# Optimization experiments

Measured on AMD Instinct MI355X. Metric: run time of the kernel, lower is better.

Reference implementation:

```python
import jax, jax.numpy as jnp
import numpy as np

B, N = 1, 1024
C_A, C_Z, H = 768, 128, 16
CH = C_A // H  # 48
INV_SQRT_CH = float(1.0 / np.sqrt(CH))


def _ln(x, w, b):
    # torch.nn.LayerNorm over last dim, eps=1e-5
    m = jnp.mean(x, axis=-1, keepdims=True)
    v = jnp.mean(jnp.square(x - m), axis=-1, keepdims=True)
    return (x - m) * jax.lax.rsqrt(v + 1e-5) * w + b


def setup_inputs() -> dict:
    key = jax.random.key(0)
    ks = jax.random.split(key, 8)
    rn = lambda k, shape, sc: jax.random.normal(k, shape, dtype=jnp.float32) * sc
    return {
        "a": rn(ks[0], (B, N, C_A), 1.0),
        "z": rn(ks[1], (B, N, N, C_Z), 1.0),
        "mask": jnp.ones((B, N), dtype=jnp.float32),
        "ln_a_w": jnp.ones((C_A,), jnp.float32),
        "ln_a_b": jnp.zeros((C_A,), jnp.float32),
        "ln_z_w": jnp.ones((C_Z,), jnp.float32),
        "ln_z_b": jnp.zeros((C_Z,), jnp.float32),
        "Wq": rn(ks[2], (C_A, H * CH), 0.02),
        "bq": jnp.zeros((H * CH,), jnp.float32),
        "Wk": rn(ks[3], (C_A, H * CH), 0.02),
        "Wv": rn(ks[4], (C_A, H * CH), 0.02),
        "Wb": rn(ks[5], (C_Z, H), 0.02),
        "Wg": rn(ks[6], (C_A, H * CH), 0.02),
        "Wo": rn(ks[7], (H * CH, C_A), 0.02),
    }


def reference(a, z, mask, ln_a_w, ln_a_b, ln_z_w, ln_z_b, Wq, bq, Wk, Wv, Wb, Wg, Wo):
    an = _ln(a, ln_a_w, ln_a_b)                                  # [B, N, C_A]
    q = (an @ Wq + bq).reshape(B, N, H, CH)
    k = (an @ Wk).reshape(B, N, H, CH)
    v = (an @ Wv).reshape(B, N, H, CH)
    # pair bias: LayerNorm(z) -> per-head scalar bias [B, N, N, H]
    bpair = _ln(z, ln_z_w, ln_z_b) @ Wb
    mbias = (mask - 1.0)[:, None, None, :] * 1e9                  # [B, 1, 1, N]
    logits = jnp.einsum('bqhc,bkhc->bhqk', q, k) * INV_SQRT_CH
    logits = logits + jnp.transpose(bpair, (0, 3, 1, 2)) + mbias  # [B, H, N, N]
    attn = jax.nn.softmax(logits, axis=-1)
    o = jnp.einsum('bhqk,bkhc->bqhc', attn, v)                    # [B, N, H, CH]
    g = jax.nn.sigmoid(an @ Wg).reshape(B, N, H, CH)
    out = (g * o).reshape(B, N, H * CH) @ Wo                      # [B, N, C_A]
    return out
```

## Files before the change

kernel.cpp:

```cpp
#include <hip/hip_runtime.h>

#define NSEQ 1024
#define CA   768
#define CZ   128
#define NH   16
#define CHD  48
#define HC   768
#define INV_SQRT_CH 0.14433756729740643f

typedef float v4f __attribute__((ext_vector_type(4)));
typedef short v8s __attribute__((ext_vector_type(8)));

__device__ __forceinline__ short f2bf(float f) {
  union { float f; unsigned u; } v; v.f = f;
  unsigned r = v.u + 0x7fffu + ((v.u >> 16) & 1u);
  return (short)(r >> 16);
}
__device__ __forceinline__ float bf2f(short s) {
  union { unsigned u; float f; } v;
  v.u = ((unsigned)(unsigned short)s) << 16;
  return v.f;
}
__device__ __forceinline__ unsigned cvtpk(float lo, float hi) {
  unsigned r;
  asm("v_cvt_pk_bf16_f32 %0, %1, %2" : "=v"(r) : "v"(lo), "v"(hi));
  return r;
}

__global__ __launch_bounds__(256) void k_front(
    const float* __restrict__ lnzw, const float* __restrict__ lnzb,
    const float* __restrict__ Wb, short* __restrict__ wWp, float* __restrict__ S1bW,
    const float* __restrict__ Wq, const float* __restrict__ Wk,
    const float* __restrict__ Wv, const float* __restrict__ Wg,
    const float* __restrict__ Wo, short* __restrict__ WT, short* __restrict__ WoT,
    const float* __restrict__ a, const float* __restrict__ lnaw,
    const float* __restrict__ lnab, short* __restrict__ anb)
{
  __shared__ __align__(16) char fsm[64 * 65 * 4];
  const int bid = blockIdx.x;
  const int t = threadIdx.x;

  if (bid == 0) {
    const int s = t >> 6, l = t & 63;
    const int r16 = l & 15, cg = l >> 4;
    float v[8];
    #pragma unroll
    for (int j = 0; j < 8; ++j) {
      int d = s * 32 + cg * 8 + j;
      v[j] = lnzw[d] * Wb[d * NH + r16];
    }
    uint4 pk;
    pk.x = cvtpk(v[0], v[1]); pk.y = cvtpk(v[2], v[3]);
    pk.z = cvtpk(v[4], v[5]); pk.w = cvtpk(v[6], v[7]);
    *(uint4*)(wWp + (s * 64 + l) * 8) = pk;
    if (t < NH) {
      float s1 = 0.f, bw = 0.f;
      for (int d = 0; d < CZ; ++d) {
        float wb = Wb[d * NH + t];
        s1 += bf2f(f2bf(lnzw[d] * wb));
        bw += lnzb[d] * wb;
      }
      S1bW[t] = s1;
      S1bW[NH + t] = bw;
    }
  } else if (bid <= 720) {
    float (*tile)[65] = (float(*)[65])fsm;
    const int cb = bid - 1;
    const int mat = cb / 144, rem = cb % 144;
    const int tk = rem % 12, tn = rem / 12;
    const int k0 = tk * 64, n0 = tn * 64;
    const float* __restrict__ W =
        (mat == 0) ? Wq : (mat == 1) ? Wk : (mat == 2) ? Wv : (mat == 3) ? Wg : Wo;
    const float s = (mat == 0) ? INV_SQRT_CH : 1.f;
    const int rr = t >> 4, cc = (t & 15) * 4;
    #pragma unroll
    for (int r = 0; r < 4; ++r) {
      v4f v = *(const v4f*)(W + (size_t)(k0 + r * 16 + rr) * HC + n0 + cc);
      tile[r * 16 + rr][cc + 0] = v[0];
      tile[r * 16 + rr][cc + 1] = v[1];
      tile[r * 16 + rr][cc + 2] = v[2];
      tile[r * 16 + rr][cc + 3] = v[3];
    }
    __syncthreads();
    short* dst = (mat < 4) ? (WT + (size_t)mat * HC * CA) : WoT;
    #pragma unroll
    for (int r = 0; r < 4; ++r) {
      const int nr = r * 16 + rr;
      uint2 pk;
      pk.x = cvtpk(tile[cc + 0][nr] * s, tile[cc + 1][nr] * s);
      pk.y = cvtpk(tile[cc + 2][nr] * s, tile[cc + 3][nr] * s);
      *(uint2*)(dst + (size_t)(n0 + nr) * CA + k0 + cc) = pk;
    }
  } else {
    float* red = (float*)fsm;
    const int row = bid - 721;
    const float* ar = a + (size_t)row * CA;
    float x[3];
    float s = 0.f, s2 = 0.f;
    #pragma unroll
    for (int i = 0; i < 3; ++i) {
      x[i] = ar[t + i * 256];
      s += x[i]; s2 += x[i] * x[i];
    }
    #pragma unroll
    for (int off = 1; off < 64; off <<= 1) {
      s += __shfl_xor(s, off);
      s2 += __shfl_xor(s2, off);
    }
    const int wv = t >> 6;
    if ((t & 63) == 0) { red[wv] = s; red[4 + wv] = s2; }
    __syncthreads();
    s = red[0] + red[1] + red[2] + red[3];
    s2 = red[4] + red[5] + red[6] + red[7];
    const float m = s * (1.f / CA);
    const float var = s2 * (1.f / CA) - m * m;
    const float rs = rsqrtf(var + 1e-5f);
    #pragma unroll
    for (int i = 0; i < 3; ++i) {
      int c = t + i * 256;
      anb[(size_t)row * CA + c] = f2bf((x[i] - m) * rs * lnaw[c] + lnab[c]);
    }
  }
}

__global__ __launch_bounds__(256) void k2_gemm(
    const short* __restrict__ anb, const short* __restrict__ WT,
    const float* __restrict__ bq,
    short* __restrict__ qb, short* __restrict__ kb, short* __restrict__ vT,
    float* __restrict__ gbuf)
{
  __shared__ __align__(16) short As[128 * 40];
  __shared__ __align__(16) short Bs[128 * 40];
  const int tid = threadIdx.x;
  const int w = tid >> 6, l = tid & 63;
  const int r16 = l & 15, cg = l >> 4;
  const int bm = blockIdx.x & 7;
  const int bnb = blockIdx.x >> 3;
  const int m0 = bm * 128, n0 = bnb * 128;
  const int wr = w >> 1, wc = w & 1;
  const int strow = w * 16 + (l >> 2);
  const int scol = (l & 3) * 8;

  v4f acc[4][4];
  #pragma unroll
  for (int i = 0; i < 4; ++i)
    #pragma unroll
    for (int j = 0; j < 4; ++j)
      acc[i][j] = (v4f){0.f, 0.f, 0.f, 0.f};

  for (int k0 = 0; k0 < CA; k0 += 32) {
    v8s av0 = *(const v8s*)(anb + (size_t)(m0 + strow) * CA + k0 + scol);
    v8s av1 = *(const v8s*)(anb + (size_t)(m0 + 64 + strow) * CA + k0 + scol);
    v8s bv0 = *(const v8s*)(WT + (size_t)(n0 + strow) * CA + k0 + scol);
    v8s bv1 = *(const v8s*)(WT + (size_t)(n0 + 64 + strow) * CA + k0 + scol);
    __syncthreads();
    *(v8s*)(As + (size_t)strow * 40 + scol) = av0;
    *(v8s*)(As + (size_t)(64 + strow) * 40 + scol) = av1;
    *(v8s*)(Bs + (size_t)strow * 40 + scol) = bv0;
    *(v8s*)(Bs + (size_t)(64 + strow) * 40 + scol) = bv1;
    __syncthreads();
    v8s a[4], b[4];
    #pragma unroll
    for (int m = 0; m < 4; ++m)
      a[m] = *(const v8s*)(As + (wr * 64 + m * 16 + r16) * 40 + cg * 8);
    #pragma unroll
    for (int n = 0; n < 4; ++n)
      b[n] = *(const v8s*)(Bs + (wc * 64 + n * 16 + r16) * 40 + cg * 8);
    #pragma unroll
    for (int m = 0; m < 4; ++m)
      #pragma unroll
      for (int n = 0; n < 4; ++n)
        acc[m][n] = __builtin_amdgcn_mfma_f32_16x16x32_bf16(a[m], b[n], acc[m][n], 0, 0, 0);
  }

  const int matsel = n0 / HC;
  #pragma unroll
  for (int n = 0; n < 4; ++n) {
    const int nc = (n0 % HC) + wc * 64 + n * 16 + r16;
    const int rbase = m0 + wr * 64 + cg * 4;
    if (matsel == 0) {
      const float bqs = bq[nc] * INV_SQRT_CH;
      #pragma unroll
      for (int m = 0; m < 4; ++m)
        #pragma unroll
        for (int j = 0; j < 4; ++j)
          qb[(size_t)(rbase + m * 16 + j) * HC + nc] = f2bf(acc[m][n][j] + bqs);
    } else if (matsel == 1) {
      #pragma unroll
      for (int m = 0; m < 4; ++m)
        #pragma unroll
        for (int j = 0; j < 4; ++j)
          kb[(size_t)(rbase + m * 16 + j) * HC + nc] = f2bf(acc[m][n][j]);
    } else if (matsel == 2) {
      #pragma unroll
      for (int m = 0; m < 4; ++m) {
        uint2 pk;
        pk.x = cvtpk(acc[m][n][0], acc[m][n][1]);
        pk.y = cvtpk(acc[m][n][2], acc[m][n][3]);
        *(uint2*)(vT + (size_t)nc * NSEQ + rbase + m * 16) = pk;
      }
    } else {
      #pragma unroll
      for (int m = 0; m < 4; ++m)
        #pragma unroll
        for (int j = 0; j < 4; ++j)
          gbuf[(size_t)(rbase + m * 16 + j) * HC + nc] =
              1.f / (1.f + __expf(-acc[m][n][j]));
    }
  }
}

__global__ __launch_bounds__(256) void k3_z(
    const float* __restrict__ z, const short* __restrict__ wWp,
    const float* __restrict__ S1bW, short* __restrict__ bpair)
{
  __shared__ __align__(16) short blds[16 * 72];
  const int tid = threadIdx.x;
  const int w = tid >> 6, l = tid & 63;
  const int r16 = l & 15, cg = l >> 4;
  const int q = blockIdx.x >> 4;
  const int k0 = (blockIdx.x & 15) << 6;

  v8s bfrag[4];
  #pragma unroll
  for (int s = 0; s < 4; ++s) bfrag[s] = *(const v8s*)(wWp + (s * 64 + l) * 8);
  const float S1 = S1bW[r16];
  const float bW = S1bW[NH + r16];

  const int krow = k0 + w * 16 + r16;
  const float* __restrict__ zr = z + ((size_t)q * NSEQ + krow) * CZ;
  float sum = 0.f, sum2 = 0.f;
  v8s afrag[4];
  #pragma unroll
  for (int s = 0; s < 4; ++s) {
    v4f z0 = *(const v4f*)(zr + s * 32 + cg * 8);
    v4f z1 = *(const v4f*)(zr + s * 32 + cg * 8 + 4);
    #pragma unroll
    for (int j = 0; j < 4; ++j) {
      sum += z0[j] + z1[j];
      sum2 += z0[j] * z0[j] + z1[j] * z1[j];
    }
    union { v8s s8; unsigned u[4]; } fu;
    fu.u[0] = cvtpk(z0[0], z0[1]);
    fu.u[1] = cvtpk(z0[2], z0[3]);
    fu.u[2] = cvtpk(z1[0], z1[1]);
    fu.u[3] = cvtpk(z1[2], z1[3]);
    afrag[s] = fu.s8;
  }
  sum  += __shfl_xor(sum, 16);  sum  += __shfl_xor(sum, 32);
  sum2 += __shfl_xor(sum2, 16); sum2 += __shfl_xor(sum2, 32);
  const float mean = sum * (1.f / CZ);
  const float var = sum2 * (1.f / CZ) - mean * mean;
  const float rs = rsqrtf(var + 1e-5f);

  v4f acc = {0.f, 0.f, 0.f, 0.f};
  #pragma unroll
  for (int s = 0; s < 4; ++s)
    acc = __builtin_amdgcn_mfma_f32_16x16x32_bf16(afrag[s], bfrag[s], acc, 0, 0, 0);

  float bv[4];
  #pragma unroll
  for (int j = 0; j < 4; ++j) {
    int src = cg * 4 + j;
    float mj = __shfl(mean, src);
    float rj = __shfl(rs, src);
    bv[j] = rj * (acc[j] - mj * S1) + bW;
  }
  uint2 bu;
  bu.x = cvtpk(bv[0], bv[1]);
  bu.y = cvtpk(bv[2], bv[3]);
  *(uint2*)&blds[r16 * 72 + w * 16 + cg * 4] = bu;
  __syncthreads();
  const int h = tid >> 4, kk = (tid & 15) << 2;
  uint2 v = *(const uint2*)&blds[h * 72 + kk];
  *(uint2*)(bpair + (size_t)h * NSEQ * NSEQ + (size_t)q * NSEQ + k0 + kk) = v;
}

#define PL_STRIDE 136
__global__ __launch_bounds__(64) void k4_attn(
    const short* __restrict__ qb, const short* __restrict__ kb,
    const short* __restrict__ vT, const short* __restrict__ bpair,
    const float* __restrict__ mask,
    float* __restrict__ po, float* __restrict__ pm, float* __restrict__ plo)
{
  const int h = blockIdx.x & 15;
  const int qt = (blockIdx.x >> 4) & 63;
  const int ks = blockIdx.x >> 10;
  const int l = threadIdx.x;
  const int r16 = l & 15, cg = l >> 4;
  const int q0 = qt * 16;
  const int k0 = ks * 128;

  __shared__ __align__(16) short pl[16 * PL_STRIDE];

  const v8s vzero = {0, 0, 0, 0, 0, 0, 0, 0};
  v8s qf0, qf1;
  {
    const short* qp = qb + (size_t)(q0 + r16) * HC + h * CHD;
    qf0 = *(const v8s*)(qp + cg * 8);
    qf1 = (cg < 2) ? *(const v8s*)(qp + 32 + cg * 8) : vzero;
  }

  const size_t bpb = (size_t)h * NSEQ * NSEQ;
  {
    const int srow = l >> 2;
    const int scol = (l & 3) * 32;
    const short* bsrc = bpair + bpb + (size_t)(q0 + srow) * NSEQ + k0 + scol;
    short* bdst = pl + srow * PL_STRIDE + scol;
    v8s t0 = *(const v8s*)(bsrc);
    v8s t1 = *(const v8s*)(bsrc + 8);
    v8s t2 = *(const v8s*)(bsrc + 16);
    v8s t3 = *(const v8s*)(bsrc + 24);
    *(v8s*)(bdst)      = t0;
    *(v8s*)(bdst + 8)  = t1;
    *(v8s*)(bdst + 16) = t2;
    *(v8s*)(bdst + 24) = t3;
  }

  v4f cs[8];
  #pragma unroll
  for (int kt = 0; kt < 8; ++kt) {
    const short* kp = kb + (size_t)(k0 + kt * 16 + r16) * HC + h * CHD;
    v8s b0 = *(const v8s*)(kp + cg * 8);
    v8s b1 = (cg < 2) ? *(const v8s*)(kp + 32 + cg * 8) : vzero;
    v4f tacc = {0.f, 0.f, 0.f, 0.f};
    tacc = __builtin_amdgcn_mfma_f32_16x16x32_bf16(qf0, b0, tacc, 0, 0, 0);
    tacc = __builtin_amdgcn_mfma_f32_16x16x32_bf16(qf1, b1, tacc, 0, 0, 0);
    cs[kt] = tacc;
  }

  #pragma unroll
  for (int kt = 0; kt < 8; ++kt) {
    const int kc = k0 + kt * 16 + r16;
    const float mb = (mask[kc] - 1.f) * 1e9f;
    #pragma unroll
    for (int j = 0; j < 4; ++j)
      cs[kt][j] += bf2f(pl[(cg * 4 + j) * PL_STRIDE + kt * 16 + r16]) + mb;
  }

  float mx4[4], ls4[4];
  #pragma unroll
  for (int j = 0; j < 4; ++j) {
    float mx = fmaxf(fmaxf(fmaxf(cs[0][j], cs[1][j]), fmaxf(cs[2][j], cs[3][j])),
                     fmaxf(fmaxf(cs[4][j], cs[5][j]), fmaxf(cs[6][j], cs[7][j])));
    mx = fmaxf(mx, __shfl_xor(mx, 1));
    mx = fmaxf(mx, __shfl_xor(mx, 2));
    mx = fmaxf(mx, __shfl_xor(mx, 4));
    mx = fmaxf(mx, __shfl_xor(mx, 8));
    mx4[j] = mx;
    float p[8];
    #pragma unroll
    for (int kt = 0; kt < 8; ++kt) p[kt] = __expf(cs[kt][j] - mx);
    float rsum = ((p[0] + p[1]) + (p[2] + p[3])) + ((p[4] + p[5]) + (p[6] + p[7]));
    rsum += __shfl_xor(rsum, 1);
    rsum += __shfl_xor(rsum, 2);
    rsum += __shfl_xor(rsum, 4);
    rsum += __shfl_xor(rsum, 8);
    ls4[j] = rsum;
    const int rowb = (cg * 4 + j) * PL_STRIDE;
    #pragma unroll
    for (int t2 = 0; t2 < 4; ++t2) {
      unsigned u = cvtpk(p[2 * t2], p[2 * t2 + 1]);
      pl[rowb + (2 * t2) * 16 + r16] = (short)u;
      pl[rowb + (2 * t2 + 1) * 16 + r16] = (short)(u >> 16);
    }
  }
  asm volatile("s_waitcnt lgkmcnt(0)" ::: "memory");
  __builtin_amdgcn_sched_barrier(0);

  v4f of0 = {0, 0, 0, 0}, of1 = {0, 0, 0, 0}, of2 = {0, 0, 0, 0};
  #pragma unroll
  for (int ks4 = 0; ks4 < 4; ++ks4) {
    v8s pa = *(const v8s*)(pl + r16 * PL_STRIDE + ks4 * 32 + cg * 8);
    const short* vp = vT + (size_t)(h * CHD + r16) * NSEQ + k0 + ks4 * 32 + cg * 8;
    v8s bv0 = *(const v8s*)vp;
    v8s bv1 = *(const v8s*)(vp + 16 * NSEQ);
    v8s bv2 = *(const v8s*)(vp + 32 * NSEQ);
    of0 = __builtin_amdgcn_mfma_f32_16x16x32_bf16(pa, bv0, of0, 0, 0, 0);
    of1 = __builtin_amdgcn_mfma_f32_16x16x32_bf16(pa, bv1, of1, 0, 0, 0);
    of2 = __builtin_amdgcn_mfma_f32_16x16x32_bf16(pa, bv2, of2, 0, 0, 0);
  }

  #pragma unroll
  for (int j = 0; j < 4; ++j) {
    const int q = q0 + cg * 4 + j;
    const size_t rb = (((size_t)ks * NSEQ + q) * NH + h) * CHD + r16;
    po[rb]      = of0[j];
    po[rb + 16] = of1[j];
    po[rb + 32] = of2[j];
    if (r16 == 0) {
      pm[((size_t)ks * NSEQ + q) * NH + h] = mx4[j];
      plo[((size_t)ks * NSEQ + q) * NH + h] = ls4[j];
    }
  }
}

__global__ __launch_bounds__(256) void kcomb(
    const float* __restrict__ po, const float* __restrict__ pm,
    const float* __restrict__ plo, const float* __restrict__ gbuf,
    short* __restrict__ gob)
{
  const int q = blockIdx.x;
  const int t = threadIdx.x;
  const int h = t >> 4, s = t & 15;
  float mi[8], li[8];
  #pragma unroll
  for (int i = 0; i < 8; ++i) {
    mi[i] = pm[((size_t)i * NSEQ + q) * NH + h];
    li[i] = plo[((size_t)i * NSEQ + q) * NH + h];
  }
  float mstar = -1e30f;
  #pragma unroll
  for (int i = 0; i < 8; ++i) mstar = fmaxf(mstar, mi[i]);
  float wgt[8], L = 0.f;
  #pragma unroll
  for (int i = 0; i < 8; ++i) { wgt[i] = __expf(mi[i] - mstar); L += li[i] * wgt[i]; }
  const float inv = 1.f / L;
  #pragma unroll
  for (int dd = 0; dd < 3; ++dd) {
    const int d = s + dd * 16;
    float o = 0.f;
    #pragma unroll
    for (int i = 0; i < 8; ++i)
      o += po[(((size_t)i * NSEQ + q) * NH + h) * CHD + d] * wgt[i];
    const float gv = gbuf[(size_t)q * HC + h * CHD + d];
    gob[(size_t)q * HC + h * CHD + d] = f2bf(o * inv * gv);
  }
}

__global__ __launch_bounds__(256) void k5_out(
    const short* __restrict__ gob, const short* __restrict__ WoT,
    float* __restrict__ out)
{
  __shared__ __align__(16) short As[64 * 40];
  __shared__ __align__(16) short Bs[64 * 40];
  const int tid = threadIdx.x;
  const int w = tid >> 6, l = tid & 63;
  const int r16 = l & 15, cg = l >> 4;
  const int bm = blockIdx.x & 15;
  const int bn = blockIdx.x >> 4;
  const int m0 = bm * 64, n0 = bn * 64;
  const int wr = w >> 1, wc = w & 1;
  const int strow = tid >> 2;
  const int scol = (tid & 3) * 8;

  v4f acc[2][2];
  #pragma unroll
  for (int i = 0; i < 2; ++i)
    #pragma unroll
    for (int j = 0; j < 2; ++j)
      acc[i][j] = (v4f){0.f, 0.f, 0.f, 0.f};

  for (int k0 = 0; k0 < CA; k0 += 32) {
    v8s av = *(const v8s*)(gob + (size_t)(m0 + strow) * CA + k0 + scol);
    v8s bv = *(const v8s*)(WoT + (size_t)(n0 + strow) * CA + k0 + scol);
    __syncthreads();
    *(v8s*)(As + (size_t)strow * 40 + scol) = av;
    *(v8s*)(Bs + (size_t)strow * 40 + scol) = bv;
    __syncthreads();
    v8s a[2], b[2];
    #pragma unroll
    for (int m = 0; m < 2; ++m)
      a[m] = *(const v8s*)(As + (wr * 32 + m * 16 + r16) * 40 + cg * 8);
    #pragma unroll
    for (int n = 0; n < 2; ++n)
      b[n] = *(const v8s*)(Bs + (wc * 32 + n * 16 + r16) * 40 + cg * 8);
    #pragma unroll
    for (int m = 0; m < 2; ++m)
      #pragma unroll
      for (int n = 0; n < 2; ++n)
        acc[m][n] = __builtin_amdgcn_mfma_f32_16x16x32_bf16(a[m], b[n], acc[m][n], 0, 0, 0);
  }

  #pragma unroll
  for (int n = 0; n < 2; ++n) {
    const int nc = n0 + wc * 32 + n * 16 + r16;
    const int rbase = m0 + wr * 32 + cg * 4;
    #pragma unroll
    for (int m = 0; m < 2; ++m)
      #pragma unroll
      for (int j = 0; j < 4; ++j)
        out[(size_t)(rbase + m * 16 + j) * CA + nc] = acc[m][n][j];
  }
}

extern "C" void kernel_launch(void* const* d_in, const int* in_sizes, int n_in,
                              void* d_out, int out_size, void* d_ws, size_t ws_size,
                              hipStream_t stream) {
  const float* a      = (const float*)d_in[0];
  const float* z      = (const float*)d_in[1];
  const float* mask   = (const float*)d_in[2];
  const float* ln_a_w = (const float*)d_in[3];
  const float* ln_a_b = (const float*)d_in[4];
  const float* ln_z_w = (const float*)d_in[5];
  const float* ln_z_b = (const float*)d_in[6];
  const float* Wq     = (const float*)d_in[7];
  const float* bq     = (const float*)d_in[8];
  const float* Wk     = (const float*)d_in[9];
  const float* Wv     = (const float*)d_in[10];
  const float* Wb     = (const float*)d_in[11];
  const float* Wg     = (const float*)d_in[12];
  const float* Wo     = (const float*)d_in[13];
  float* out = (float*)d_out;

  char* ws = (char*)d_ws;
  short* anb   = (short*)(ws);
  short* WT    = (short*)(ws + (2ull << 20));
  short* WoT   = (short*)(ws + (7ull << 20));
  short* qb    = (short*)(ws + (9ull << 20));
  short* kb    = (short*)(ws + (11ull << 20));
  short* vT    = (short*)(ws + (13ull << 20));
  float* gbuf  = (float*)(ws + (15ull << 20));
  short* wWp   = (short*)(ws + (19ull << 20));
  float* S1bW  = (float*)(ws + (19ull << 20) + 4096ull);
  short* gob   = (short*)(ws + (20ull << 20));
  float* po    = (float*)(ws + (22ull << 20));
  float* pm    = (float*)(ws + (48ull << 20));
  float* plo   = (float*)(ws + (49ull << 20));
  short* bpair = (short*)(ws + (50ull << 20));

  k_front<<<1745, 256, 0, stream>>>(ln_z_w, ln_z_b, Wb, wWp, S1bW,
                                    Wq, Wk, Wv, Wg, Wo, WT, WoT,
                                    a, ln_a_w, ln_a_b, anb);
  k2_gemm<<<192, 256, 0, stream>>>(anb, WT, bq, qb, kb, vT, gbuf);
  k3_z<<<16384, 256, 0, stream>>>(z, wWp, S1bW, bpair);
  k4_attn<<<8192, 64, 0, stream>>>(qb, kb, vT, bpair, mask, po, pm, plo);
  kcomb<<<1024, 256, 0, stream>>>(po, pm, plo, gbuf, gob);
  k5_out<<<192, 256, 0, stream>>>(gob, WoT, out);
}
```

Baseline: 198.4 us.

## Fuse split-K attention combine into attention kernel via LDS; loop k3 over tiles

The attention kernel now runs all eight key splits as eight waves of one 512-thread block. Each wave writes its partial outputs, max and sum into LDS, and the block merges them and applies the gate in place. This removes the separate combine kernel and the global round-trip of the fp32 partials. Separately, the z-projection kernel now handles four 64-key tiles per block in a loop, cutting its grid to a quarter. The trade-off is heavy LDS use per attention block, which lowers occupancy, plus an extra barrier per tile in k3.

```diff
diff --git a/kernel.cpp b/kernel.cpp
--- a/kernel.cpp
+++ b/kernel.cpp
@@ -218,80 +218,88 @@
   const int tid = threadIdx.x;
   const int w = tid >> 6, l = tid & 63;
   const int r16 = l & 15, cg = l >> 4;
-  const int q = blockIdx.x >> 4;
-  const int k0 = (blockIdx.x & 15) << 6;
+  const int q = blockIdx.x >> 2;
+  const int kq = (blockIdx.x & 3) << 8;
 
   v8s bfrag[4];
   #pragma unroll
   for (int s = 0; s < 4; ++s) bfrag[s] = *(const v8s*)(wWp + (s * 64 + l) * 8);
   const float S1 = S1bW[r16];
   const float bW = S1bW[NH + r16];
-
-  const int krow = k0 + w * 16 + r16;
-  const float* __restrict__ zr = z + ((size_t)q * NSEQ + krow) * CZ;
-  float sum = 0.f, sum2 = 0.f;
-  v8s afrag[4];
-  #pragma unroll
-  for (int s = 0; s < 4; ++s) {
-    v4f z0 = *(const v4f*)(zr + s * 32 + cg * 8);
-    v4f z1 = *(const v4f*)(zr + s * 32 + cg * 8 + 4);
+  const int h = tid >> 4, kk = (tid & 15) << 2;
+
+  for (int kt = 0; kt < 4; ++kt) {
+    const int k0 = kq + kt * 64;
+    const int krow = k0 + w * 16 + r16;
+    const float* __restrict__ zr = z + ((size_t)q * NSEQ + krow) * CZ;
+    float sum = 0.f, sum2 = 0.f;
+    v8s afrag[4];
+    #pragma unroll
+    for (int s = 0; s < 4; ++s) {
+      v4f z0 = *(const v4f*)(zr + s * 32 + cg * 8);
+      v4f z1 = *(const v4f*)(zr + s * 32 + cg * 8 + 4);
+      #pragma unroll
+      for (int j = 0; j < 4; ++j) {
+        sum += z0[j] + z1[j];
+        sum2 += z0[j] * z0[j] + z1[j] * z1[j];
+      }
+      union { v8s s8; unsigned u[4]; } fu;
+      fu.u[0] = cvtpk(z0[0], z0[1]);
+      fu.u[1] = cvtpk(z0[2], z0[3]);
+      fu.u[2] = cvtpk(z1[0], z1[1]);
+      fu.u[3] = cvtpk(z1[2], z1[3]);
+      afrag[s] = fu.s8;
+    }
+    sum  += __shfl_xor(sum, 16);  sum  += __shfl_xor(sum, 32);
+    sum2 += __shfl_xor(sum2, 16); sum2 += __shfl_xor(sum2, 32);
+    const float mean = sum * (1.f / CZ);
+    const float var = sum2 * (1.f / CZ) - mean * mean;
+    const float rs = rsqrtf(var + 1e-5f);
+
+    v4f acc = {0.f, 0.f, 0.f, 0.f};
+    #pragma unroll
+    for (int s = 0; s < 4; ++s)
+      acc = __builtin_amdgcn_mfma_f32_16x16x32_bf16(afrag[s], bfrag[s], acc, 0, 0, 0);
+
+    float bv[4];
     #pragma unroll
     for (int j = 0; j < 4; ++j) {
-      sum += z0[j] + z1[j];
-      sum2 += z0[j] * z0[j] + z1[j] * z1[j];
-    }
-    union { v8s s8; unsigned u[4]; } fu;
-    fu.u[0] = cvtpk(z0[0], z0[1]);
-    fu.u[1] = cvtpk(z0[2], z0[3]);
-    fu.u[2] = cvtpk(z1[0], z1[1]);
-    fu.u[3] = cvtpk(z1[2], z1[3]);
-    afrag[s] = fu.s8;
-  }
-  sum  += __shfl_xor(sum, 16);  sum  += __shfl_xor(sum, 32);
-  sum2 += __shfl_xor(sum2, 16); sum2 += __shfl_xor(sum2, 32);
-  const float mean = sum * (1.f / CZ);
-  const float var = sum2 * (1.f / CZ) - mean * mean;
-  const float rs = rsqrtf(var + 1e-5f);
-
-  v4f acc = {0.f, 0.f, 0.f, 0.f};
-  #pragma unroll
-  for (int s = 0; s < 4; ++s)
-    acc = __builtin_amdgcn_mfma_f32_16x16x32_bf16(afrag[s], bfrag[s], acc, 0, 0, 0);
-
-  float bv[4];
-  #pragma unroll
-  for (int j = 0; j < 4; ++j) {
-    int src = cg * 4 + j;
-    float mj = __shfl(mean, src);
-    float rj = __shfl(rs, src);
-    bv[j] = rj * (acc[j] - mj * S1) + bW;
-  }
-  uint2 bu;
-  bu.x = cvtpk(bv[0], bv[1]);
-  bu.y = cvtpk(bv[2], bv[3]);
-  *(uint2*)&blds[r16 * 72 + w * 16 + cg * 4] = bu;
-  __syncthreads();
-  const int h = tid >> 4, kk = (tid & 15) << 2;
-  uint2 v = *(const uint2*)&blds[h * 72 + kk];
-  *(uint2*)(bpair + (size_t)h * NSEQ * NSEQ + (size_t)q * NSEQ + k0 + kk) = v;
+      int src = cg * 4 + j;
+      float mj = __shfl(mean, src);
+      float rj = __shfl(rs, src);
+      bv[j] = rj * (acc[j] - mj * S1) + bW;
+    }
+    uint2 bu;
+    bu.x = cvtpk(bv[0], bv[1]);
+    bu.y = cvtpk(bv[2], bv[3]);
+    *(uint2*)&blds[r16 * 72 + w * 16 + cg * 4] = bu;
+    __syncthreads();
+    uint2 v = *(const uint2*)&blds[h * 72 + kk];
+    *(uint2*)(bpair + (size_t)h * NSEQ * NSEQ + (size_t)q * NSEQ + k0 + kk) = v;
+    __syncthreads();
+  }
 }
 
 #define PL_STRIDE 136
-__global__ __launch_bounds__(64) void k4_attn(
+#define PO_STRIDE 52
+__global__ __launch_bounds__(512) void k45_attn(
     const short* __restrict__ qb, const short* __restrict__ kb,
     const short* __restrict__ vT, const short* __restrict__ bpair,
-    const float* __restrict__ mask,
-    float* __restrict__ po, float* __restrict__ pm, float* __restrict__ plo)
+    const float* __restrict__ mask, const float* __restrict__ gbuf,
+    short* __restrict__ gob)
 {
   const int h = blockIdx.x & 15;
-  const int qt = (blockIdx.x >> 4) & 63;
-  const int ks = blockIdx.x >> 10;
-  const int l = threadIdx.x;
+  const int qt = blockIdx.x >> 4;
+  const int tid = threadIdx.x;
+  const int w = tid >> 6, l = tid & 63;
   const int r16 = l & 15, cg = l >> 4;
   const int q0 = qt * 16;
-  const int k0 = ks * 128;
-
-  __shared__ __align__(16) short pl[16 * PL_STRIDE];
+  const int k0 = w * 128;
+
+  __shared__ __align__(16) short plds[8][16 * PL_STRIDE];
+  __shared__ __align__(16) float po_lds[8][16][PO_STRIDE];
+  __shared__ __align__(16) float ml_lds[8][16][2];
+  short* pl = &plds[w][0];
 
   const v8s vzero = {0, 0, 0, 0, 0, 0, 0, 0};
   v8s qf0, qf1;
@@ -383,48 +391,49 @@
 
   #pragma unroll
   for (int j = 0; j < 4; ++j) {
-    const int q = q0 + cg * 4 + j;
-    const size_t rb = (((size_t)ks * NSEQ + q) * NH + h) * CHD + r16;
-    po[rb]      = of0[j];
-    po[rb + 16] = of1[j];
-    po[rb + 32] = of2[j];
+    const int row = cg * 4 + j;
+    po_lds[w][row][r16]      = of0[j];
+    po_lds[w][row][16 + r16] = of1[j];
+    po_lds[w][row][32 + r16] = of2[j];
     if (r16 == 0) {
-      pm[((size_t)ks * NSEQ + q) * NH + h] = mx4[j];
-      plo[((size_t)ks * NSEQ + q) * NH + h] = ls4[j];
-    }
-  }
-}
-
-__global__ __launch_bounds__(256) void kcomb(
-    const float* __restrict__ po, const float* __restrict__ pm,
-    const float* __restrict__ plo, const float* __restrict__ gbuf,
-    short* __restrict__ gob)
-{
-  const int q = blockIdx.x;
-  const int t = threadIdx.x;
-  const int h = t >> 4, s = t & 15;
-  float mi[8], li[8];
-  #pragma unroll
-  for (int i = 0; i < 8; ++i) {
-    mi[i] = pm[((size_t)i * NSEQ + q) * NH + h];
-    li[i] = plo[((size_t)i * NSEQ + q) * NH + h];
-  }
-  float mstar = -1e30f;
-  #pragma unroll
-  for (int i = 0; i < 8; ++i) mstar = fmaxf(mstar, mi[i]);
-  float wgt[8], L = 0.f;
-  #pragma unroll
-  for (int i = 0; i < 8; ++i) { wgt[i] = __expf(mi[i] - mstar); L += li[i] * wgt[i]; }
-  const float inv = 1.f / L;
-  #pragma unroll
-  for (int dd = 0; dd < 3; ++dd) {
-    const int d = s + dd * 16;
-    float o = 0.f;
-    #pragma unroll
-    for (int i = 0; i < 8; ++i)
-      o += po[(((size_t)i * NSEQ + q) * NH + h) * CHD + d] * wgt[i];
-    const float gv = gbuf[(size_t)q * HC + h * CHD + d];
-    gob[(size_t)q * HC + h * CHD + d] = f2bf(o * inv * gv);
+      ml_lds[w][row][0] = mx4[j];
+      ml_lds[w][row][1] = ls4[j];
+    }
+  }
+  __syncthreads();
+
+  {
+    const int g = tid >> 5;
+    const int lane = tid & 31;
+    float mi[8], li[8];
+    #pragma unroll
+    for (int i = 0; i < 8; ++i) {
+      mi[i] = ml_lds[i][g][0];
+      li[i] = ml_lds[i][g][1];
+    }
+    float mstar = -1e30f;
+    #pragma unroll
+    for (int i = 0; i < 8; ++i) mstar = fmaxf(mstar, mi[i]);
+    float wgt[8], L = 0.f;
+    #pragma unroll
+    for (int i = 0; i < 8; ++i) { wgt[i] = __expf(mi[i] - mstar); L += li[i] * wgt[i]; }
+    const float inv = 1.f / L;
+    const int q = q0 + g;
+    {
+      float o = 0.f;
+      #pragma unroll
+      for (int i = 0; i < 8; ++i) o += po_lds[i][g][lane] * wgt[i];
+      const float gv = gbuf[(size_t)q * HC + h * CHD + lane];
+      gob[(size_t)q * HC + h * CHD + lane] = f2bf(o * inv * gv);
+    }
+    if (lane < 16) {
+      const int d = 32 + lane;
+      float o = 0.f;
+      #pragma unroll
+      for (int i = 0; i < 8; ++i) o += po_lds[i][g][d] * wgt[i];
+      const float gv = gbuf[(size_t)q * HC + h * CHD + d];
+      gob[(size_t)q * HC + h * CHD + d] = f2bf(o * inv * gv);
+    }
   }
 }
 
@@ -514,17 +523,13 @@
   short* wWp   = (short*)(ws + (19ull << 20));
   float* S1bW  = (float*)(ws + (19ull << 20) + 4096ull);
   short* gob   = (short*)(ws + (20ull << 20));
-  float* po    = (float*)(ws + (22ull << 20));
-  float* pm    = (float*)(ws + (48ull << 20));
-  float* plo   = (float*)(ws + (49ull << 20));
-  short* bpair = (short*)(ws + (50ull << 20));
+  short* bpair = (short*)(ws + (22ull << 20));
 
   k_front<<<1745, 256, 0, stream>>>(ln_z_w, ln_z_b, Wb, wWp, S1bW,
                                     Wq, Wk, Wv, Wg, Wo, WT, WoT,
                                     a, ln_a_w, ln_a_b, anb);
   k2_gemm<<<192, 256, 0, stream>>>(anb, WT, bq, qb, kb, vT, gbuf);
-  k3_z<<<16384, 256, 0, stream>>>(z, wWp, S1bW, bpair);
-  k4_attn<<<8192, 64, 0, stream>>>(qb, kb, vT, bpair, mask, po, pm, plo);
-  kcomb<<<1024, 256, 0, stream>>>(po, pm, plo, gbuf, gob);
+  k3_z<<<4096, 256, 0, stream>>>(z, wWp, S1bW, bpair);
+  k45_attn<<<1024, 512, 0, stream>>>(qb, kb, vT, bpair, mask, gbuf, gob);
   k5_out<<<192, 256, 0, stream>>>(gob, WoT, out);
 }
```

After: 194.8 us. About the same (-1.8%).
